# Kernel tuning notes

Hardware: AMD Instinct MI355X
Metric: run time of the kernel (lower is better)

Reference implementation:

```python
import jax, jax.numpy as jnp
import numpy as np

B, N, D, K = 4, 8192, 128, 32
LN_EPS = 1e-5


def setup_inputs() -> dict:
    key = jax.random.key(0)
    k1, k2, k3, k4 = jax.random.split(key, 4)
    x = jax.random.normal(k1, (B, N, D), dtype=jnp.float32)
    adj = jax.random.randint(k2, (B, N, K), 0, N, dtype=jnp.int64)
    W = jax.random.normal(k3, (2 * D, D), dtype=jnp.float32) * (1.0 / np.sqrt(2 * D))
    b = jnp.zeros((D,), dtype=jnp.float32)
    gamma = jnp.ones((D,), dtype=jnp.float32)
    beta = jnp.zeros((D,), dtype=jnp.float32)
    return {"x": x, "adj": adj, "W": W, "b": b, "gamma": gamma, "beta": beta}


def reference(x, adj, W, b, gamma, beta):
    # Gather neighbor features: neigh[b,n,k,:] = x[b, adj[b,n,k], :]
    # (avoids the original's (B,N,N,D) blowup; direct index gather)
    neigh = jnp.take_along_axis(x[:, None, :, :], adj[..., None], axis=2)  # (B,N,K,D)
    neigh_mean = neigh.mean(axis=2)  # (B,N,D)
    h = jnp.concatenate([x, neigh_mean], axis=-1)  # (B,N,2D)
    h = jnp.einsum('bnf,fd->bnd', h, W) + b
    h = jax.nn.gelu(h, approximate=False)
    # dropout is identity in eval mode
    y = h + x
    mu = y.mean(axis=-1, keepdims=True)
    var = y.var(axis=-1, keepdims=True)
    return (y - mu) * jax.lax.rsqrt(var + LN_EPS) * gamma + beta
```

## Files before the change

### kernel.cpp

```cpp
#include <hip/hip_runtime.h>

#define B_ 4
#define N_ 8192
#define D_ 128
#define K_ 32
#define BM 64
#define THREADS 512

typedef short short8 __attribute__((ext_vector_type(8)));
typedef float f32x4 __attribute__((ext_vector_type(4)));

__device__ __forceinline__ unsigned short f2bf(float f) {
  unsigned int u = __float_as_uint(f);
  u += 0x7FFFu + ((u >> 16) & 1u);
  return (unsigned short)(u >> 16);
}
__device__ __forceinline__ float bf2f(unsigned short h) {
  return __uint_as_float(((unsigned int)h) << 16);
}

__global__ __launch_bounds__(256) void cvt_kernel(const float4* __restrict__ x,
                                                  ushort4* __restrict__ xh, int n4) {
  int i = blockIdx.x * blockDim.x + threadIdx.x;
  if (i < n4) {
    float4 v = x[i];
    ushort4 o;
    o.x = f2bf(v.x); o.y = f2bf(v.y); o.z = f2bf(v.z); o.w = f2bf(v.w);
    xh[i] = o;
  }
}

template<bool USE_BF16>
__global__ __launch_bounds__(THREADS, 4) void fused_kernel(
    const float* __restrict__ x, const int* __restrict__ adj,
    const float* __restrict__ W, const float* __restrict__ bias,
    const float* __restrict__ gamma, const float* __restrict__ beta,
    const unsigned short* __restrict__ xh, float* __restrict__ out) {

  __shared__ __align__(16) unsigned char in_tile[BM * 512];
  __shared__ __align__(16) float y_lds[BM][D_];
  __shared__ int adj_lds[BM * K_];

  const int t    = threadIdx.x;
  const int wave = t >> 6;
  const int lane = t & 63;
  const int l15  = lane & 15;
  const int kg   = lane >> 4;

  const int  bidx = blockIdx.x >> 7;
  const int  n0   = (blockIdx.x & 127) * BM;
  const long row0 = (long)bidx * N_ + n0;

  const int dl = (wave << 4) + l15;
  short8 bw[8];
  #pragma unroll
  for (int ks = 0; ks < 8; ++ks) {
    #pragma unroll
    for (int j = 0; j < 8; ++j) {
      int f = ks * 32 + kg * 8 + j;
      bw[ks][j] = (short)f2bf(W[f * D_ + dl]);
    }
  }

  #pragma unroll
  for (int i = 0; i < (BM * K_) / THREADS; ++i)
    adj_lds[t + i * THREADS] = adj[row0 * K_ + t + i * THREADS];

  if constexpr (USE_BF16) {
    #pragma unroll
    for (int i = 0; i < 2; ++i) {
      int idx = t + i * THREADS;
      int row = idx >> 4;
      int cp  = (idx & 15) * 8;
      uint4 v = *reinterpret_cast<const uint4*>(xh + (row0 + row) * D_ + cp);
      *reinterpret_cast<uint4*>(in_tile + row * 512 + ((2 * cp) ^ ((row & 7) << 4))) = v;
    }
  } else {
    #pragma unroll
    for (int i = 0; i < 4; ++i) {
      int idx = t + i * THREADS;
      int row = idx >> 5;
      int cp  = (idx & 31) * 4;
      float4 v = *reinterpret_cast<const float4*>(x + (row0 + row) * D_ + cp);
      ushort4 o;
      o.x = f2bf(v.x); o.y = f2bf(v.y); o.z = f2bf(v.z); o.w = f2bf(v.w);
      *reinterpret_cast<ushort4*>(in_tile + row * 512 + ((2 * cp) ^ ((row & 7) << 4))) = o;
    }
  }
  __syncthreads();

  {
    const int g  = t & 31;
    const int rb = t >> 5;
    const int c0 = g * 4;
    #pragma unroll
    for (int batch = 0; batch < 4; ++batch) {
      int row = rb + batch * 16;
      const int* ap = adj_lds + row * K_;
      float a0 = 0.f, a1 = 0.f, a2 = 0.f, a3 = 0.f;
      #pragma unroll 8
      for (int k = 0; k < K_; ++k) {
        int a = ap[k];
        if constexpr (USE_BF16) {
          ushort4 v = *reinterpret_cast<const ushort4*>(xh + ((long)bidx * N_ + a) * D_ + c0);
          a0 += bf2f(v.x); a1 += bf2f(v.y); a2 += bf2f(v.z); a3 += bf2f(v.w);
        } else {
          float4 v = *reinterpret_cast<const float4*>(x + ((long)bidx * N_ + a) * D_ + c0);
          a0 += v.x; a1 += v.y; a2 += v.z; a3 += v.w;
        }
      }
      ushort4 m;
      m.x = f2bf(a0 * 0.03125f); m.y = f2bf(a1 * 0.03125f);
      m.z = f2bf(a2 * 0.03125f); m.w = f2bf(a3 * 0.03125f);
      *reinterpret_cast<ushort4*>(in_tile + row * 512 +
                                  ((2 * (D_ + c0)) ^ ((row & 7) << 4))) = m;
    }
  }
  __syncthreads();

  f32x4 acc[4];
  #pragma unroll
  for (int r = 0; r < 4; ++r) acc[r] = (f32x4){0.f, 0.f, 0.f, 0.f};
  #pragma unroll
  for (int ks = 0; ks < 8; ++ks) {
    #pragma unroll
    for (int r = 0; r < 4; ++r) {
      int row = r * 16 + l15;
      int f0  = ks * 32 + kg * 8;
      short8 af = *reinterpret_cast<const short8*>(
          in_tile + row * 512 + ((2 * f0) ^ ((row & 7) << 4)));
      acc[r] = __builtin_amdgcn_mfma_f32_16x16x32_bf16(af, bw[ks], acc[r], 0, 0, 0);
    }
  }

  const float bv = bias[dl];
  #pragma unroll
  for (int r = 0; r < 4; ++r) {
    #pragma unroll
    for (int i = 0; i < 4; ++i) {
      int row = r * 16 + kg * 4 + i;
      float h  = acc[r][i] + bv;
      float ge = 0.5f * h * (1.f + erff(h * 0.70710678118f));
      y_lds[row][dl] = ge + x[(row0 + row) * D_ + dl];
    }
  }
  __syncthreads();

  {
    const int row = t >> 3;
    const int l8  = t & 7;
    const float* yr = &y_lds[row][l8 * 16];
    float4 v[4];
    float s = 0.f, sq = 0.f;
    #pragma unroll
    for (int i = 0; i < 4; ++i) {
      v[i] = *reinterpret_cast<const float4*>(yr + i * 4);
      s  += v[i].x + v[i].y + v[i].z + v[i].w;
      sq += v[i].x * v[i].x + v[i].y * v[i].y + v[i].z * v[i].z + v[i].w * v[i].w;
    }
    #pragma unroll
    for (int off = 1; off < 8; off <<= 1) {
      s  += __shfl_xor(s, off, 64);
      sq += __shfl_xor(sq, off, 64);
    }
    const float mu   = s * (1.f / 128.f);
    const float rstd = rsqrtf(sq * (1.f / 128.f) - mu * mu + 1e-5f);
    float* orow = out + (row0 + row) * D_ + l8 * 16;
    #pragma unroll
    for (int i = 0; i < 4; ++i) {
      float4 g  = *reinterpret_cast<const float4*>(gamma + l8 * 16 + i * 4);
      float4 bb = *reinterpret_cast<const float4*>(beta  + l8 * 16 + i * 4);
      float4 o;
      o.x = (v[i].x - mu) * rstd * g.x + bb.x;
      o.y = (v[i].y - mu) * rstd * g.y + bb.y;
      o.z = (v[i].z - mu) * rstd * g.z + bb.z;
      o.w = (v[i].w - mu) * rstd * g.w + bb.w;
      *reinterpret_cast<float4*>(orow + i * 4) = o;
    }
  }
}

extern "C" void kernel_launch(void* const* d_in, const int* in_sizes, int n_in,
                              void* d_out, int out_size, void* d_ws, size_t ws_size,
                              hipStream_t stream) {
  const float* x     = (const float*)d_in[0];
  const int*   adj   = (const int*)d_in[1];
  const float* W     = (const float*)d_in[2];
  const float* bias  = (const float*)d_in[3];
  const float* gamma = (const float*)d_in[4];
  const float* beta  = (const float*)d_in[5];
  float* out = (float*)d_out;

  const size_t xh_bytes = (size_t)B_ * N_ * D_ * 2;
  const int nblocks = (B_ * N_) / BM;

  if (ws_size >= xh_bytes) {
    unsigned short* xh = (unsigned short*)d_ws;
    const int n4 = B_ * N_ * D_ / 4;
    cvt_kernel<<<dim3(n4 / 256), dim3(256), 0, stream>>>((const float4*)x, (ushort4*)xh, n4);
    fused_kernel<true><<<dim3(nblocks), dim3(THREADS), 0, stream>>>(
        x, adj, W, bias, gamma, beta, xh, out);
  } else {
    fused_kernel<false><<<dim3(nblocks), dim3(THREADS), 0, stream>>>(
        x, adj, W, bias, gamma, beta, nullptr, out);
  }
}
```

Baseline: 116.8 us.

## Pre-transpose W to bf16, alias LDS buffers, widen gather, remap blocks by batch

The conversion kernel now also writes a transposed bf16 copy of W, so the fused kernel loads B fragments per k-step as one 16-byte read instead of holding 64 registers of converted weights. LDS shrinks by aliasing the y buffer onto the input tile (with padded stride 132 and an extra barrier), and launch bounds rise to 8 waves-per-EU hint for higher occupancy. The neighbour gather reads 8 bf16 per load instead of 4, and block indices are swizzled so concurrently running blocks span different batches. Risks include an extra barrier and repeated W loads from global/L2 inside the MFMA loop.

Result: no change. 116.8 us (-0.0%).

```diff
diff --git a/kernel.cpp b/kernel.cpp
--- a/kernel.cpp
+++ b/kernel.cpp
@@ -6,6 +6,9 @@
 #define K_ 32
 #define BM 64
 #define THREADS 512
+#define N4X (B_ * N_ * D_ / 4)
+#define NW (2 * D_ * D_)
+#define YSTR 132
 
 typedef short short8 __attribute__((ext_vector_type(8)));
 typedef float f32x4 __attribute__((ext_vector_type(4)));
@@ -20,26 +23,36 @@
 }
 
 __global__ __launch_bounds__(256) void cvt_kernel(const float4* __restrict__ x,
-                                                  ushort4* __restrict__ xh, int n4) {
-  int i = blockIdx.x * blockDim.x + threadIdx.x;
-  if (i < n4) {
+                                                  ushort4* __restrict__ xh,
+                                                  const float* __restrict__ W,
+                                                  unsigned short* __restrict__ Wt) {
+  int i = blockIdx.x * 256 + threadIdx.x;
+  if (i < N4X) {
     float4 v = x[i];
     ushort4 o;
     o.x = f2bf(v.x); o.y = f2bf(v.y); o.z = f2bf(v.z); o.w = f2bf(v.w);
     xh[i] = o;
+  } else {
+    int e = i - N4X;
+    if (e < NW) {
+      int f = e >> 7, d = e & 127;
+      Wt[d * 256 + f] = f2bf(W[e]);
+    }
   }
 }
 
 template<bool USE_BF16>
-__global__ __launch_bounds__(THREADS, 4) void fused_kernel(
+__global__ __launch_bounds__(THREADS, 8) void fused_kernel(
     const float* __restrict__ x, const int* __restrict__ adj,
     const float* __restrict__ W, const float* __restrict__ bias,
     const float* __restrict__ gamma, const float* __restrict__ beta,
-    const unsigned short* __restrict__ xh, float* __restrict__ out) {
-
-  __shared__ __align__(16) unsigned char in_tile[BM * 512];
-  __shared__ __align__(16) float y_lds[BM][D_];
-  __shared__ int adj_lds[BM * K_];
+    const unsigned short* __restrict__ xh, const unsigned short* __restrict__ Wt,
+    float* __restrict__ out) {
+
+  __shared__ __align__(16) unsigned char smem[40960];
+  unsigned char* in_tile = smem;
+  int* adj_lds = (int*)(smem + 32768);
+  float* y = (float*)smem;
 
   const int t    = threadIdx.x;
   const int wave = t >> 6;
@@ -47,20 +60,10 @@
   const int l15  = lane & 15;
   const int kg   = lane >> 4;
 
-  const int  bidx = blockIdx.x >> 7;
-  const int  n0   = (blockIdx.x & 127) * BM;
+  const int  vid  = (blockIdx.x & 7) * 64 + (blockIdx.x >> 3);
+  const int  bidx = vid >> 7;
+  const int  n0   = (vid & 127) * BM;
   const long row0 = (long)bidx * N_ + n0;
-
-  const int dl = (wave << 4) + l15;
-  short8 bw[8];
-  #pragma unroll
-  for (int ks = 0; ks < 8; ++ks) {
-    #pragma unroll
-    for (int j = 0; j < 8; ++j) {
-      int f = ks * 32 + kg * 8 + j;
-      bw[ks][j] = (short)f2bf(W[f * D_ + dl]);
-    }
-  }
 
   #pragma unroll
   for (int i = 0; i < (BM * K_) / THREADS; ++i)
@@ -89,7 +92,31 @@
   }
   __syncthreads();
 
-  {
+  if constexpr (USE_BF16) {
+    const int g16 = t & 15;
+    const int rb  = t >> 4;
+    const int c0  = g16 * 8;
+    #pragma unroll
+    for (int half = 0; half < 2; ++half) {
+      int row = rb + half * 32;
+      const int* ap = adj_lds + row * K_;
+      float a[8] = {0.f, 0.f, 0.f, 0.f, 0.f, 0.f, 0.f, 0.f};
+      #pragma unroll 8
+      for (int k = 0; k < K_; ++k) {
+        uint4 v = *reinterpret_cast<const uint4*>(
+            xh + ((long)bidx * N_ + ap[k]) * D_ + c0);
+        const unsigned short* pv = (const unsigned short*)&v;
+        #pragma unroll
+        for (int j = 0; j < 8; ++j) a[j] += bf2f(pv[j]);
+      }
+      unsigned short m[8];
+      #pragma unroll
+      for (int j = 0; j < 8; ++j) m[j] = f2bf(a[j] * 0.03125f);
+      *reinterpret_cast<uint4*>(in_tile + row * 512 +
+                                ((256 + 2 * c0) ^ ((row & 7) << 4))) =
+          *reinterpret_cast<uint4*>(m);
+    }
+  } else {
     const int g  = t & 31;
     const int rb = t >> 5;
     const int c0 = g * 4;
@@ -100,14 +127,9 @@
       float a0 = 0.f, a1 = 0.f, a2 = 0.f, a3 = 0.f;
       #pragma unroll 8
       for (int k = 0; k < K_; ++k) {
-        int a = ap[k];
-        if constexpr (USE_BF16) {
-          ushort4 v = *reinterpret_cast<const ushort4*>(xh + ((long)bidx * N_ + a) * D_ + c0);
-          a0 += bf2f(v.x); a1 += bf2f(v.y); a2 += bf2f(v.z); a3 += bf2f(v.w);
-        } else {
-          float4 v = *reinterpret_cast<const float4*>(x + ((long)bidx * N_ + a) * D_ + c0);
-          a0 += v.x; a1 += v.y; a2 += v.z; a3 += v.w;
-        }
+        float4 v = *reinterpret_cast<const float4*>(
+            x + ((long)bidx * N_ + ap[k]) * D_ + c0);
+        a0 += v.x; a1 += v.y; a2 += v.z; a3 += v.w;
       }
       ushort4 m;
       m.x = f2bf(a0 * 0.03125f); m.y = f2bf(a1 * 0.03125f);
@@ -118,20 +140,29 @@
   }
   __syncthreads();
 
+  const int dl = (wave << 4) + l15;
   f32x4 acc[4];
   #pragma unroll
   for (int r = 0; r < 4; ++r) acc[r] = (f32x4){0.f, 0.f, 0.f, 0.f};
   #pragma unroll
   for (int ks = 0; ks < 8; ++ks) {
+    short8 bwk;
+    if constexpr (USE_BF16) {
+      bwk = *reinterpret_cast<const short8*>(Wt + dl * 256 + ks * 32 + kg * 8);
+    } else {
+      #pragma unroll
+      for (int j = 0; j < 8; ++j)
+        bwk[j] = (short)f2bf(W[(ks * 32 + kg * 8 + j) * D_ + dl]);
+    }
     #pragma unroll
     for (int r = 0; r < 4; ++r) {
       int row = r * 16 + l15;
-      int f0  = ks * 32 + kg * 8;
       short8 af = *reinterpret_cast<const short8*>(
-          in_tile + row * 512 + ((2 * f0) ^ ((row & 7) << 4)));
-      acc[r] = __builtin_amdgcn_mfma_f32_16x16x32_bf16(af, bw[ks], acc[r], 0, 0, 0);
-    }
-  }
+          in_tile + row * 512 + ((2 * (ks * 32 + kg * 8)) ^ ((row & 7) << 4)));
+      acc[r] = __builtin_amdgcn_mfma_f32_16x16x32_bf16(af, bwk, acc[r], 0, 0, 0);
+    }
+  }
+  __syncthreads();
 
   const float bv = bias[dl];
   #pragma unroll
@@ -141,7 +172,7 @@
       int row = r * 16 + kg * 4 + i;
       float h  = acc[r][i] + bv;
       float ge = 0.5f * h * (1.f + erff(h * 0.70710678118f));
-      y_lds[row][dl] = ge + x[(row0 + row) * D_ + dl];
+      y[row * YSTR + dl] = ge + x[(row0 + row) * D_ + dl];
     }
   }
   __syncthreads();
@@ -149,7 +180,7 @@
   {
     const int row = t >> 3;
     const int l8  = t & 7;
-    const float* yr = &y_lds[row][l8 * 16];
+    const float* yr = y + row * YSTR + l8 * 16;
     float4 v[4];
     float s = 0.f, sq = 0.f;
     #pragma unroll
@@ -192,16 +223,18 @@
   float* out = (float*)d_out;
 
   const size_t xh_bytes = (size_t)B_ * N_ * D_ * 2;
+  const size_t wt_bytes = (size_t)NW * 2;
   const int nblocks = (B_ * N_) / BM;
 
-  if (ws_size >= xh_bytes) {
+  if (ws_size >= xh_bytes + wt_bytes) {
     unsigned short* xh = (unsigned short*)d_ws;
-    const int n4 = B_ * N_ * D_ / 4;
-    cvt_kernel<<<dim3(n4 / 256), dim3(256), 0, stream>>>((const float4*)x, (ushort4*)xh, n4);
+    unsigned short* Wt = (unsigned short*)((char*)d_ws + xh_bytes);
+    const int ncvt = (N4X + NW + 255) / 256;
+    cvt_kernel<<<dim3(ncvt), dim3(256), 0, stream>>>((const float4*)x, (ushort4*)xh, W, Wt);
     fused_kernel<true><<<dim3(nblocks), dim3(THREADS), 0, stream>>>(
-        x, adj, W, bias, gamma, beta, xh, out);
+        x, adj, W, bias, gamma, beta, xh, Wt, out);
   } else {
     fused_kernel<false><<<dim3(nblocks), dim3(THREADS), 0, stream>>>(
-        x, adj, W, bias, gamma, beta, nullptr, out);
-  }
-}
+        x, adj, W, bias, gamma, beta, nullptr, nullptr, out);
+  }
+}
```

## Apply linear layer before the neighbor gather, then gather projected rows

Applied to the files above, without the earlier changes.

Because the mean and the matmul are both linear, mean(x[adj]) @ W_bottom equals mean((x @ W_bottom)[adj]). A GEMM kernel now computes x@W_top in fp32 and x@W_bottom in bf16 into the workspace. A gather kernel then averages the projected bf16 rows per node and applies bias, GELU, the residual and LayerNorm with one wave per node. The fallback fused kernel also gets an XCD-aware block swizzle, a padded LDS stride and per-step W loads. The cost is extra workspace traffic, since p1 is written and read in fp32, and rounding the projected neighbor values to bf16 changes the numerics.

Result: faster. 110.3 us (-5.6%).

```diff
diff --git a/kernel.cpp b/kernel.cpp
--- a/kernel.cpp
+++ b/kernel.cpp
@@ -4,8 +4,6 @@
 #define N_ 8192
 #define D_ 128
 #define K_ 32
-#define BM 64
-#define THREADS 512
 
 typedef short short8 __attribute__((ext_vector_type(8)));
 typedef float f32x4 __attribute__((ext_vector_type(4)));
@@ -19,95 +17,160 @@
   return __uint_as_float(((unsigned int)h) << 16);
 }
 
-__global__ __launch_bounds__(256) void cvt_kernel(const float4* __restrict__ x,
-                                                  ushort4* __restrict__ xh, int n4) {
-  int i = blockIdx.x * blockDim.x + threadIdx.x;
-  if (i < n4) {
-    float4 v = x[i];
+__global__ __launch_bounds__(512) void gemm_kernel(
+    const float* __restrict__ x, const float* __restrict__ W,
+    float* __restrict__ p1, unsigned short* __restrict__ p2h) {
+  __shared__ __align__(16) unsigned char in_tile[32 * 256];
+
+  const int t = threadIdx.x, wave = t >> 6, lane = t & 63;
+  const int l15 = lane & 15, kg = lane >> 4;
+  const long row0 = (long)blockIdx.x * 32;
+
+  #pragma unroll
+  for (int i = 0; i < 2; ++i) {
+    int idx = t + i * 512;
+    int row = idx >> 5, cs = idx & 31;
+    float4 v = *reinterpret_cast<const float4*>(x + (row0 + row) * D_ + cs * 4);
     ushort4 o;
     o.x = f2bf(v.x); o.y = f2bf(v.y); o.z = f2bf(v.z); o.w = f2bf(v.w);
-    xh[i] = o;
-  }
-}
-
-template<bool USE_BF16>
-__global__ __launch_bounds__(THREADS, 4) void fused_kernel(
+    *reinterpret_cast<ushort4*>(
+        in_tile + ((row * 256 + cs * 8) ^ ((row & 7) << 4))) = o;
+  }
+
+  const int halfw = wave & 3, is_v = wave >> 2;
+  const float* Wb = W + (is_v ? D_ * D_ : 0);
+  short8 bw[2][4];
+  #pragma unroll
+  for (int tt = 0; tt < 2; ++tt)
+    #pragma unroll
+    for (int ks = 0; ks < 4; ++ks)
+      #pragma unroll
+      for (int j = 0; j < 8; ++j)
+        bw[tt][ks][j] = (short)f2bf(
+            Wb[(ks * 32 + kg * 8 + j) * D_ + halfw * 32 + tt * 16 + l15]);
+  __syncthreads();
+
+  f32x4 acc[2][2];
+  #pragma unroll
+  for (int r = 0; r < 2; ++r)
+    #pragma unroll
+    for (int tt = 0; tt < 2; ++tt)
+      acc[r][tt] = (f32x4){0.f, 0.f, 0.f, 0.f};
+
+  #pragma unroll
+  for (int ks = 0; ks < 4; ++ks) {
+    #pragma unroll
+    for (int r = 0; r < 2; ++r) {
+      int row = r * 16 + l15;
+      short8 af = *reinterpret_cast<const short8*>(
+          in_tile + ((row * 256 + ks * 64 + kg * 16) ^ ((row & 7) << 4)));
+      acc[r][0] = __builtin_amdgcn_mfma_f32_16x16x32_bf16(af, bw[0][ks], acc[r][0], 0, 0, 0);
+      acc[r][1] = __builtin_amdgcn_mfma_f32_16x16x32_bf16(af, bw[1][ks], acc[r][1], 0, 0, 0);
+    }
+  }
+
+  #pragma unroll
+  for (int r = 0; r < 2; ++r)
+    #pragma unroll
+    for (int tt = 0; tt < 2; ++tt)
+      #pragma unroll
+      for (int i = 0; i < 4; ++i) {
+        int row = r * 16 + kg * 4 + i;
+        int col = halfw * 32 + tt * 16 + l15;
+        float val = acc[r][tt][i];
+        if (!is_v) p1[(row0 + row) * D_ + col] = val;
+        else       p2h[(row0 + row) * D_ + col] = f2bf(val);
+      }
+}
+
+__global__ __launch_bounds__(256) void gather_kernel(
+    const int* __restrict__ adj, const float* __restrict__ p1,
+    const unsigned short* __restrict__ p2h, const float* __restrict__ x,
+    const float* __restrict__ bias, const float* __restrict__ gamma,
+    const float* __restrict__ beta, float* __restrict__ out) {
+  const int t = threadIdx.x;
+  const int wave = t >> 6, lane = t & 63;
+  const int vblk = ((blockIdx.x & 7) << 8) + (blockIdx.x >> 3);
+  const int node_base = vblk * 16 + wave * 4;
+  const int b = node_base >> 13;
+  const unsigned int* vb =
+      (const unsigned int*)p2h + (size_t)b * (N_ * (D_ / 2));
+  const int c0 = lane * 2;
+  const float2 bi = *reinterpret_cast<const float2*>(bias + c0);
+  const float2 ga = *reinterpret_cast<const float2*>(gamma + c0);
+  const float2 be = *reinterpret_cast<const float2*>(beta + c0);
+  const int nbu = __builtin_amdgcn_readfirstlane(node_base);
+
+  #pragma unroll
+  for (int j = 0; j < 4; ++j) {
+    const int gn = nbu + j;
+    const int* ap = adj + (size_t)gn * K_;
+    float a0 = 0.f, a1 = 0.f;
+    #pragma unroll
+    for (int k = 0; k < K_; ++k) {
+      unsigned int v = vb[(size_t)ap[k] * (D_ / 2) + lane];
+      a0 += __uint_as_float(v << 16);
+      a1 += __uint_as_float(v & 0xFFFF0000u);
+    }
+    const float2 u  = *reinterpret_cast<const float2*>(p1 + (size_t)gn * D_ + c0);
+    const float2 xv = *reinterpret_cast<const float2*>(x  + (size_t)gn * D_ + c0);
+    float h0 = u.x + a0 * 0.03125f + bi.x;
+    float h1 = u.y + a1 * 0.03125f + bi.y;
+    h0 = 0.5f * h0 * (1.f + erff(h0 * 0.70710678118f));
+    h1 = 0.5f * h1 * (1.f + erff(h1 * 0.70710678118f));
+    const float y0 = h0 + xv.x, y1 = h1 + xv.y;
+    float s = y0 + y1, sq = y0 * y0 + y1 * y1;
+    #pragma unroll
+    for (int off = 1; off < 64; off <<= 1) {
+      s  += __shfl_xor(s, off, 64);
+      sq += __shfl_xor(sq, off, 64);
+    }
+    const float mu   = s * (1.f / 128.f);
+    const float rstd = rsqrtf(sq * (1.f / 128.f) - mu * mu + 1e-5f);
+    float2 o;
+    o.x = (y0 - mu) * rstd * ga.x + be.x;
+    o.y = (y1 - mu) * rstd * ga.y + be.y;
+    *reinterpret_cast<float2*>(out + (size_t)gn * D_ + c0) = o;
+  }
+}
+
+__global__ __launch_bounds__(512) void fused_f32_kernel(
     const float* __restrict__ x, const int* __restrict__ adj,
     const float* __restrict__ W, const float* __restrict__ bias,
     const float* __restrict__ gamma, const float* __restrict__ beta,
-    const unsigned short* __restrict__ xh, float* __restrict__ out) {
-
-  __shared__ __align__(16) unsigned char in_tile[BM * 512];
-  __shared__ __align__(16) float y_lds[BM][D_];
-  __shared__ int adj_lds[BM * K_];
-
-  const int t    = threadIdx.x;
-  const int wave = t >> 6;
-  const int lane = t & 63;
-  const int l15  = lane & 15;
-  const int kg   = lane >> 4;
-
-  const int  bidx = blockIdx.x >> 7;
-  const int  n0   = (blockIdx.x & 127) * BM;
-  const long row0 = (long)bidx * N_ + n0;
-
-  const int dl = (wave << 4) + l15;
-  short8 bw[8];
-  #pragma unroll
-  for (int ks = 0; ks < 8; ++ks) {
-    #pragma unroll
-    for (int j = 0; j < 8; ++j) {
-      int f = ks * 32 + kg * 8 + j;
-      bw[ks][j] = (short)f2bf(W[f * D_ + dl]);
-    }
-  }
-
-  #pragma unroll
-  for (int i = 0; i < (BM * K_) / THREADS; ++i)
-    adj_lds[t + i * THREADS] = adj[row0 * K_ + t + i * THREADS];
-
-  if constexpr (USE_BF16) {
-    #pragma unroll
-    for (int i = 0; i < 2; ++i) {
-      int idx = t + i * THREADS;
-      int row = idx >> 4;
-      int cp  = (idx & 15) * 8;
-      uint4 v = *reinterpret_cast<const uint4*>(xh + (row0 + row) * D_ + cp);
-      *reinterpret_cast<uint4*>(in_tile + row * 512 + ((2 * cp) ^ ((row & 7) << 4))) = v;
-    }
-  } else {
-    #pragma unroll
-    for (int i = 0; i < 4; ++i) {
-      int idx = t + i * THREADS;
-      int row = idx >> 5;
-      int cp  = (idx & 31) * 4;
-      float4 v = *reinterpret_cast<const float4*>(x + (row0 + row) * D_ + cp);
-      ushort4 o;
-      o.x = f2bf(v.x); o.y = f2bf(v.y); o.z = f2bf(v.z); o.w = f2bf(v.w);
-      *reinterpret_cast<ushort4*>(in_tile + row * 512 + ((2 * cp) ^ ((row & 7) << 4))) = o;
-    }
-  }
-  __syncthreads();
-
+    float* __restrict__ out) {
+  __shared__ __align__(16) unsigned char smem[40960];
+  unsigned char* in_tile = smem;
+  int* adj_lds = (int*)(smem + 32768);
+  float* y = (float*)smem;
+  const int t = threadIdx.x, wave = t >> 6, lane = t & 63;
+  const int l15 = lane & 15, kg = lane >> 4;
+  const int vid = (blockIdx.x & 7) * 64 + (blockIdx.x >> 3);
+  const int bidx = vid >> 7;
+  const long row0 = (long)bidx * N_ + (vid & 127) * 64;
+  #pragma unroll
+  for (int i = 0; i < 4; ++i)
+    adj_lds[t + i * 512] = adj[row0 * K_ + t + i * 512];
+  #pragma unroll
+  for (int i = 0; i < 4; ++i) {
+    int idx = t + i * 512;
+    int row = idx >> 5, cp = (idx & 31) * 4;
+    float4 v = *reinterpret_cast<const float4*>(x + (row0 + row) * D_ + cp);
+    ushort4 o;
+    o.x = f2bf(v.x); o.y = f2bf(v.y); o.z = f2bf(v.z); o.w = f2bf(v.w);
+    *reinterpret_cast<ushort4*>(in_tile + row * 512 + ((2 * cp) ^ ((row & 7) << 4))) = o;
+  }
+  __syncthreads();
   {
-    const int g  = t & 31;
-    const int rb = t >> 5;
-    const int c0 = g * 4;
+    const int g = t & 31, rb = t >> 5, c0 = g * 4;
     #pragma unroll
     for (int batch = 0; batch < 4; ++batch) {
       int row = rb + batch * 16;
       const int* ap = adj_lds + row * K_;
-      float a0 = 0.f, a1 = 0.f, a2 = 0.f, a3 = 0.f;
-      #pragma unroll 8
+      float a0 = 0, a1 = 0, a2 = 0, a3 = 0;
       for (int k = 0; k < K_; ++k) {
-        int a = ap[k];
-        if constexpr (USE_BF16) {
-          ushort4 v = *reinterpret_cast<const ushort4*>(xh + ((long)bidx * N_ + a) * D_ + c0);
-          a0 += bf2f(v.x); a1 += bf2f(v.y); a2 += bf2f(v.z); a3 += bf2f(v.w);
-        } else {
-          float4 v = *reinterpret_cast<const float4*>(x + ((long)bidx * N_ + a) * D_ + c0);
-          a0 += v.x; a1 += v.y; a2 += v.z; a3 += v.w;
-        }
+        float4 v = *reinterpret_cast<const float4*>(x + ((long)bidx * N_ + ap[k]) * D_ + c0);
+        a0 += v.x; a1 += v.y; a2 += v.z; a3 += v.w;
       }
       ushort4 m;
       m.x = f2bf(a0 * 0.03125f); m.y = f2bf(a1 * 0.03125f);
@@ -117,59 +180,59 @@
     }
   }
   __syncthreads();
-
+  const int dl = (wave << 4) + l15;
   f32x4 acc[4];
   #pragma unroll
   for (int r = 0; r < 4; ++r) acc[r] = (f32x4){0.f, 0.f, 0.f, 0.f};
   #pragma unroll
   for (int ks = 0; ks < 8; ++ks) {
+    short8 bwk;
+    #pragma unroll
+    for (int j = 0; j < 8; ++j)
+      bwk[j] = (short)f2bf(W[(ks * 32 + kg * 8 + j) * D_ + dl]);
     #pragma unroll
     for (int r = 0; r < 4; ++r) {
       int row = r * 16 + l15;
-      int f0  = ks * 32 + kg * 8;
       short8 af = *reinterpret_cast<const short8*>(
-          in_tile + row * 512 + ((2 * f0) ^ ((row & 7) << 4)));
-      acc[r] = __builtin_amdgcn_mfma_f32_16x16x32_bf16(af, bw[ks], acc[r], 0, 0, 0);
-    }
-  }
-
+          in_tile + row * 512 + ((2 * (ks * 32 + kg * 8)) ^ ((row & 7) << 4)));
+      acc[r] = __builtin_amdgcn_mfma_f32_16x16x32_bf16(af, bwk, acc[r], 0, 0, 0);
+    }
+  }
+  __syncthreads();
   const float bv = bias[dl];
   #pragma unroll
-  for (int r = 0; r < 4; ++r) {
+  for (int r = 0; r < 4; ++r)
     #pragma unroll
     for (int i = 0; i < 4; ++i) {
       int row = r * 16 + kg * 4 + i;
-      float h  = acc[r][i] + bv;
+      float h = acc[r][i] + bv;
       float ge = 0.5f * h * (1.f + erff(h * 0.70710678118f));
-      y_lds[row][dl] = ge + x[(row0 + row) * D_ + dl];
-    }
-  }
-  __syncthreads();
-
+      y[row * 132 + dl] = ge + x[(row0 + row) * D_ + dl];
+    }
+  __syncthreads();
   {
-    const int row = t >> 3;
-    const int l8  = t & 7;
-    const float* yr = &y_lds[row][l8 * 16];
+    const int row = t >> 3, l8 = t & 7;
+    const float* yr = y + row * 132 + l8 * 16;
     float4 v[4];
     float s = 0.f, sq = 0.f;
     #pragma unroll
     for (int i = 0; i < 4; ++i) {
       v[i] = *reinterpret_cast<const float4*>(yr + i * 4);
-      s  += v[i].x + v[i].y + v[i].z + v[i].w;
+      s += v[i].x + v[i].y + v[i].z + v[i].w;
       sq += v[i].x * v[i].x + v[i].y * v[i].y + v[i].z * v[i].z + v[i].w * v[i].w;
     }
     #pragma unroll
     for (int off = 1; off < 8; off <<= 1) {
-      s  += __shfl_xor(s, off, 64);
+      s += __shfl_xor(s, off, 64);
       sq += __shfl_xor(sq, off, 64);
     }
-    const float mu   = s * (1.f / 128.f);
+    const float mu = s * (1.f / 128.f);
     const float rstd = rsqrtf(sq * (1.f / 128.f) - mu * mu + 1e-5f);
     float* orow = out + (row0 + row) * D_ + l8 * 16;
     #pragma unroll
     for (int i = 0; i < 4; ++i) {
-      float4 g  = *reinterpret_cast<const float4*>(gamma + l8 * 16 + i * 4);
-      float4 bb = *reinterpret_cast<const float4*>(beta  + l8 * 16 + i * 4);
+      float4 g = *reinterpret_cast<const float4*>(gamma + l8 * 16 + i * 4);
+      float4 bb = *reinterpret_cast<const float4*>(beta + l8 * 16 + i * 4);
       float4 o;
       o.x = (v[i].x - mu) * rstd * g.x + bb.x;
       o.y = (v[i].y - mu) * rstd * g.y + bb.y;
@@ -191,17 +254,17 @@
   const float* beta  = (const float*)d_in[5];
   float* out = (float*)d_out;
 
-  const size_t xh_bytes = (size_t)B_ * N_ * D_ * 2;
-  const int nblocks = (B_ * N_) / BM;
-
-  if (ws_size >= xh_bytes) {
-    unsigned short* xh = (unsigned short*)d_ws;
-    const int n4 = B_ * N_ * D_ / 4;
-    cvt_kernel<<<dim3(n4 / 256), dim3(256), 0, stream>>>((const float4*)x, (ushort4*)xh, n4);
-    fused_kernel<true><<<dim3(nblocks), dim3(THREADS), 0, stream>>>(
-        x, adj, W, bias, gamma, beta, xh, out);
+  const size_t p1_bytes = (size_t)B_ * N_ * D_ * 4;
+  const size_t p2_bytes = (size_t)B_ * N_ * D_ * 2;
+
+  if (ws_size >= p1_bytes + p2_bytes) {
+    float* p1 = (float*)d_ws;
+    unsigned short* p2h = (unsigned short*)((char*)d_ws + p1_bytes);
+    gemm_kernel<<<dim3((B_ * N_) / 32), dim3(512), 0, stream>>>(x, W, p1, p2h);
+    gather_kernel<<<dim3(2048), dim3(256), 0, stream>>>(
+        adj, p1, p2h, x, bias, gamma, beta, out);
   } else {
-    fused_kernel<false><<<dim3(nblocks), dim3(THREADS), 0, stream>>>(
-        x, adj, W, bias, gamma, beta, nullptr, out);
-  }
-}
+    fused_f32_kernel<<<dim3((B_ * N_) / 64), dim3(512), 0, stream>>>(
+        x, adj, W, bias, gamma, beta, out);
+  }
+}
```
